# Performance work log

Hardware: AMD Instinct MI355X
Metric: run time of the kernel (lower is better)

Reference implementation:

```python
import jax, jax.numpy as jnp
import numpy as np

B, S, D = 2, 1024, 4096          # batch, prefill seqlen, model dim
H, KVH, HD = 32, 8, 128          # q heads, kv heads, head dim
MAX = 2048                       # kv-cache capacity
THETA = 1000000.0
REP = H // KVH


def _rope_tables(pos):
    # pos: [S] int -> cos/sin [S, HD]
    inv_freq = 1.0 / (THETA ** (jnp.arange(0, HD, 2, dtype=jnp.float32) / HD))
    freqs = pos[:, None].astype(jnp.float32) * inv_freq[None, :]
    emb = jnp.concatenate([freqs, freqs], axis=-1)
    return jnp.cos(emb), jnp.sin(emb)


def _rotate_half(t):
    t1, t2 = jnp.split(t, 2, axis=-1)
    return jnp.concatenate([-t2, t1], axis=-1)


def setup_inputs() -> dict:
    key = jax.random.key(0)
    k = jax.random.split(key, 8)
    sc = 1.0 / np.sqrt(D)
    x = jax.random.normal(k[0], (B, S, D), jnp.float32)
    storage_idx = jnp.arange(S, dtype=jnp.int32)
    cache = jnp.zeros((2, 1, B, KVH, MAX, HD), jnp.float32)
    causal = jnp.tril(jnp.ones((MAX, MAX), bool))
    mask = jnp.where(causal, 0.0, -1e9).astype(jnp.float32)
    Wq = jax.random.normal(k[1], (D, H * HD), jnp.float32) * sc
    bq = jax.random.normal(k[2], (H * HD,), jnp.float32) * 0.01
    Wk = jax.random.normal(k[3], (D, KVH * HD), jnp.float32) * sc
    bk = jax.random.normal(k[4], (KVH * HD,), jnp.float32) * 0.01
    Wv = jax.random.normal(k[5], (D, KVH * HD), jnp.float32) * sc
    bv = jax.random.normal(k[6], (KVH * HD,), jnp.float32) * 0.01
    Wo = jax.random.normal(k[7], (H * HD, D), jnp.float32) * sc
    return {"x": x, "storage_idx": storage_idx, "cache": cache, "mask": mask,
            "Wq": Wq, "bq": bq, "Wk": Wk, "bk": bk, "Wv": Wv, "bv": bv, "Wo": Wo}


def reference(x, storage_idx, cache, mask, Wq, bq, Wk, bk, Wv, bv, Wo):
    bsz, seqlen, _ = x.shape
    # QKV projections -> [b, heads, s, hd]
    xq = (x @ Wq + bq).reshape(bsz, seqlen, H, HD).transpose(0, 2, 1, 3)
    xk = (x @ Wk + bk).reshape(bsz, seqlen, KVH, HD).transpose(0, 2, 1, 3)
    xv = (x @ Wv + bv).reshape(bsz, seqlen, KVH, HD).transpose(0, 2, 1, 3)
    # inline RoPE at positions storage_idx
    cos, sin = _rope_tables(storage_idx)       # [s, hd]
    cos = cos[None, None]                      # [1,1,s,hd]
    sin = sin[None, None]
    xq = xq * cos + _rotate_half(xq) * sin
    xk = xk * cos + _rotate_half(xk) * sin
    # KV-cache scatter (index_copy_ on dim -2 at storage_idx)
    keys = cache[0, 0].at[:, :, storage_idx, :].set(xk)    # [b, kvh, MAX, hd]
    values = cache[1, 0].at[:, :, storage_idx, :].set(xv)
    # GQA: repeat kv heads
    keys = jnp.repeat(keys, REP, axis=1)       # [b, H, MAX, hd]
    values = jnp.repeat(values, REP, axis=1)
    # attention with additive mask rows gathered at storage_idx
    scores = jnp.einsum('bhqd,bhkd->bhqk', xq, keys) / np.sqrt(HD)
    scores = scores + mask[storage_idx][None, None]        # [b, H, s, MAX]
    attn = jax.nn.softmax(scores, axis=-1)
    out = jnp.einsum('bhqk,bhkd->bhqd', attn, values)
    out = out.transpose(0, 2, 1, 3).reshape(bsz, seqlen, H * HD)
    return out @ Wo
```

## Files before the change

kernel.cpp:

```cpp
#include <hip/hip_runtime.h>
#include <hip/hip_bf16.h>

typedef unsigned short u16;
typedef unsigned int   u32;
using bf16x8 = __attribute__((ext_vector_type(8))) short;
using f32x4  = __attribute__((ext_vector_type(4))) float;

#define AS1 __attribute__((address_space(1)))
#define AS3 __attribute__((address_space(3)))

static constexpr int S_   = 1024;
static constexpr int D_   = 4096;
static constexpr int H_   = 32;
static constexpr int KVH_ = 8;
static constexpr int HD_  = 128;
static constexpr int NQKV = H_*HD_ + 2*KVH_*HD_;

__device__ __forceinline__ u16 f2bf(float f) {
  union { float f; u32 u; } v; v.f = f;
  u32 r = v.u + 0x7FFFu + ((v.u >> 16) & 1u);
  return (u16)(r >> 16);
}

__global__ void k_convert(const float* __restrict__ src, u16* __restrict__ dst, int n4) {
  int i = blockIdx.x * blockDim.x + threadIdx.x;
  if (i >= n4) return;
  float4 v = ((const float4*)src)[i];
  ushort4 o;
  o.x = f2bf(v.x); o.y = f2bf(v.y); o.z = f2bf(v.z); o.w = f2bf(v.w);
  ((ushort4*)dst)[i] = o;
}

__global__ void k_transpose_w(const float* __restrict__ src, u16* __restrict__ dst,
                              int K, int N) {
  __shared__ float t[32][33];
  int k0 = blockIdx.y * 32, n0 = blockIdx.x * 32;
  int tx = threadIdx.x, ty = threadIdx.y;
#pragma unroll
  for (int i = 0; i < 4; ++i)
    t[ty + i*8][tx] = src[(size_t)(k0 + ty + i*8) * N + n0 + tx];
  __syncthreads();
#pragma unroll
  for (int i = 0; i < 4; ++i)
    dst[(size_t)(n0 + ty + i*8) * K + k0 + tx] = f2bf(t[tx][ty + i*8]);
}

__global__ void k_transpose_v(const u16* __restrict__ src, u16* __restrict__ dst) {
  __shared__ u16 t[32][33];
  int bg = blockIdx.z;
  int s0 = blockIdx.x * 32, h0 = blockIdx.y * 32;
  src += (size_t)bg * S_ * HD_;
  dst += (size_t)bg * S_ * HD_;
  int tx = threadIdx.x, ty = threadIdx.y;
#pragma unroll
  for (int i = 0; i < 4; ++i)
    t[ty + i*8][tx] = src[(size_t)(s0 + ty + i*8) * HD_ + h0 + tx];
  __syncthreads();
#pragma unroll
  for (int i = 0; i < 4; ++i)
    dst[(size_t)(h0 + ty + i*8) * S_ + s0 + tx] = t[tx][ty + i*8];
}

__global__ void k_rope(const int* __restrict__ sidx, float* __restrict__ cosd,
                       float* __restrict__ sind) {
  int i = blockIdx.x * blockDim.x + threadIdx.x;
  int s = i >> 6, d = i & 63;
  float pos  = (float)sidx[s];
  float invf = expf(-0.21586735246819178f * (float)d);
  float ph   = pos * invf;
  cosd[i] = cosf(ph);
  sind[i] = sinf(ph);
}

__global__ __launch_bounds__(512, 2) void k_gemmq(
    const u16* __restrict__ A, const u16* __restrict__ Bt,
    const float* __restrict__ bq, const float* __restrict__ bk,
    const float* __restrict__ bv,
    const float* __restrict__ cosd, const float* __restrict__ sind,
    u16* __restrict__ qb, u16* __restrict__ kb, u16* __restrict__ vb)
{
  constexpr int K = 4096;
  constexpr int ABYT = 256*128, BBYT = 256*128, STEP = ABYT+BBYT;
  __shared__ __align__(16) char lds[2*STEP];

  const int cpx = (int)gridDim.x >> 3;
  const int wkid = ((int)blockIdx.x & 7)*cpx + ((int)blockIdx.x >> 3);
  const int NT = 24;
  const int m0 = (wkid / NT) * 256, n0 = (wkid % NT) * 256;
  const int tid = threadIdx.x, w = tid>>6, lane = tid&63;
  const int l15 = lane&15, l4 = lane>>4;
  const int wr = w>>1, wc = w&1;
  const int row0 = tid>>3;
  const int ss = (tid&7) ^ (row0&7);
  const int NK = K >> 6;

  f32x4 acc[4][8];
#pragma unroll
  for (int i = 0; i < 4; ++i)
#pragma unroll
    for (int j = 0; j < 8; ++j) acc[i][j] = (f32x4){0.f,0.f,0.f,0.f};

  bf16x8 af[2][2];
  bf16x8 bfr[2][4][2];

#define QCHUNK(kt_, part_, r0c_)                                              \
  __builtin_amdgcn_global_load_lds(                                           \
    (AS1 void*)(((part_) ? Bt + (size_t)(n0 + (r0c_) + row0)*K                \
                         : A  + (size_t)(m0 + (r0c_) + row0)*K)               \
                + (size_t)(kt_)*64 + ss*8),                                   \
    (AS3 void*)(lds + ((kt_)&1)*STEP + (part_)*ABYT + (r0c_)*128 + w*1024),   \
    16, 0, 0)

#define QLOAD_A(mh_)                                                          \
  _Pragma("unroll") for (int i2 = 0; i2 < 2; ++i2)                            \
  _Pragma("unroll") for (int kk = 0; kk < 2; ++kk) {                          \
    int row = wr*64 + ((mh_)*2 + i2)*16 + l15;                                \
    af[i2][kk] = *(const bf16x8*)(lA + row*128 + (((kk*4+l4) ^ (row&7)) << 4)); }

#define QLOAD_B(nh_)                                                          \
  _Pragma("unroll") for (int jj = 0; jj < 4; ++jj)                            \
  _Pragma("unroll") for (int kk = 0; kk < 2; ++kk) {                          \
    int row = wc*128 + ((nh_)*4 + jj)*16 + l15;                               \
    bfr[nh_][jj][kk] = *(const bf16x8*)(lB + row*128 + (((kk*4+l4) ^ (row&7)) << 4)); }

#define QMFMA(mh_, nh_)                                                       \
  __builtin_amdgcn_s_setprio(1);                                              \
  _Pragma("unroll") for (int i2 = 0; i2 < 2; ++i2)                            \
  _Pragma("unroll") for (int jj = 0; jj < 4; ++jj)                            \
  _Pragma("unroll") for (int kk = 0; kk < 2; ++kk)                            \
    acc[(mh_)*2+i2][(nh_)*4+jj] = __builtin_amdgcn_mfma_f32_16x16x32_bf16(    \
        af[i2][kk], bfr[nh_][jj][kk], acc[(mh_)*2+i2][(nh_)*4+jj], 0, 0, 0);  \
  __builtin_amdgcn_s_setprio(0);

#define BAR   __builtin_amdgcn_s_barrier()
#define SCHB  __builtin_amdgcn_sched_barrier(0)
#define WLGKM asm volatile("s_waitcnt lgkmcnt(0)" ::: "memory")

  QCHUNK(0,0,0); QCHUNK(0,0,64); QCHUNK(0,0,128); QCHUNK(0,0,192);
  QCHUNK(0,1,0); QCHUNK(0,1,64); QCHUNK(0,1,128); QCHUNK(0,1,192);
  QCHUNK(1,0,0); QCHUNK(1,0,64); QCHUNK(1,0,128); QCHUNK(1,0,192);
  QCHUNK(1,1,0); QCHUNK(1,1,64); QCHUNK(1,1,128); QCHUNK(1,1,192);
  asm volatile("s_waitcnt vmcnt(8)" ::: "memory");
  BAR; SCHB;

  for (int kt = 0; kt < NK; ++kt) {
    const char* lA = lds + (kt&1)*STEP;
    const char* lB = lA + ABYT;
    QLOAD_A(0); QLOAD_B(0);
    BAR; WLGKM; SCHB;
    QMFMA(0,0);
    BAR;
    QLOAD_B(1);
    BAR; WLGKM; SCHB;
    QMFMA(0,1);
    BAR;
    QLOAD_A(1);
    if (kt+2 < NK) { QCHUNK(kt+2,1,0); QCHUNK(kt+2,1,64); QCHUNK(kt+2,1,128); QCHUNK(kt+2,1,192); }
    BAR; WLGKM; SCHB;
    QMFMA(1,0);
    BAR;
    if (kt+2 < NK) {
      QCHUNK(kt+2,0,0); QCHUNK(kt+2,0,64); QCHUNK(kt+2,0,128); QCHUNK(kt+2,0,192);
      asm volatile("s_waitcnt vmcnt(8)" ::: "memory");
    } else {
      asm volatile("s_waitcnt vmcnt(0)" ::: "memory");
    }
    BAR; WLGKM; SCHB;
    QMFMA(1,1);
    BAR;
  }
#undef QCHUNK
#undef QLOAD_A
#undef QLOAD_B
#undef QMFMA

  const int btype = (n0 >= H_*HD_) + (n0 >= H_*HD_ + KVH_*HD_);
  const int colbase = n0 + wc*128 - (btype==1 ? H_*HD_ : btype==2 ? H_*HD_+KVH_*HD_ : 0);
  const int hloc = colbase >> 7;
  const float* bias = btype==0 ? bq : btype==1 ? bk : bv;
  u16* dst = btype==0 ? qb : btype==1 ? kb : vb;
  const int nheads = btype==0 ? H_ : KVH_;
  const float scale = btype==0 ? 0.08838834764831845f : 1.0f;

  float bb[8];
#pragma unroll
  for (int j = 0; j < 8; ++j) bb[j] = bias[colbase + j*16 + l15];

#pragma unroll
  for (int i = 0; i < 4; ++i)
#pragma unroll
    for (int r = 0; r < 4; ++r) {
      int sr = m0 + wr*64 + i*16 + l4*4 + r;
      int b_ = sr >> 10, s_ = sr & 1023;
      size_t obase = (((size_t)b_*nheads + hloc)*S_ + s_)*(size_t)HD_;
      if (btype < 2) {
#pragma unroll
        for (int j = 0; j < 4; ++j) {
          float cs = cosd[s_*64 + j*16 + l15];
          float sn = sind[s_*64 + j*16 + l15];
          float lo = acc[i][j][r]   + bb[j];
          float hi = acc[i][j+4][r] + bb[j+4];
          dst[obase + j*16 + l15]      = f2bf((lo*cs - hi*sn) * scale);
          dst[obase + 64 + j*16 + l15] = f2bf((hi*cs + lo*sn) * scale);
        }
      } else {
#pragma unroll
        for (int j = 0; j < 8; ++j)
          dst[obase + j*16 + l15] = f2bf(acc[i][j][r] + bb[j]);
      }
    }
}

template<int BN>
__global__ __launch_bounds__(512, 2) void k_gemm3(
    const u16* __restrict__ A, const u16* __restrict__ Bt,
    float* __restrict__ C, int N, int K)
{
  constexpr int WN = BN/4, NJ = WN/16, NH = NJ/2;
  constexpr int ABYT = 256*128, BBYT = BN*128, STEP = ABYT+BBYT;
  __shared__ __align__(16) char lds[2*STEP];

  const int cpx = (int)gridDim.x >> 3;
  const int wkid = ((int)blockIdx.x & 7)*cpx + ((int)blockIdx.x >> 3);
  const int NT = N / BN;
  const int m0 = (wkid / NT) * 256, n0 = (wkid % NT) * BN;
  const int tid = threadIdx.x, w = tid>>6, lane = tid&63;
  const int l15 = lane&15, l4 = lane>>4;
  const int wr = w>>2, wc = w&3;
  const int row0 = tid>>3;
  const int ss = (tid&7) ^ (row0&7);
  const int NK = K >> 6;

  f32x4 acc[8][NJ];
#pragma unroll
  for (int i = 0; i < 8; ++i)
#pragma unroll
    for (int j = 0; j < NJ; ++j) acc[i][j] = (f32x4){0.f,0.f,0.f,0.f};

  bf16x8 af[4][2];
  bf16x8 bf[2][NH][2];

#define CHUNK(kt_, part_, r0c_)                                               \
  __builtin_amdgcn_global_load_lds(                                           \
    (AS1 void*)(((part_) ? Bt + (size_t)(n0 + (r0c_) + row0)*K                \
                         : A  + (size_t)(m0 + (r0c_) + row0)*K)               \
                + (size_t)(kt_)*64 + ss*8),                                   \
    (AS3 void*)(lds + ((kt_)&1)*STEP + (part_)*ABYT + (r0c_)*128 + w*1024),   \
    16, 0, 0)

#define LOAD_A(mh_)                                                           \
  _Pragma("unroll") for (int i = 0; i < 4; ++i)                               \
  _Pragma("unroll") for (int kk = 0; kk < 2; ++kk) {                          \
    int row = wr*128 + (mh_)*64 + i*16 + l15;                                 \
    af[i][kk] = *(const bf16x8*)(lA + row*128 + (((kk*4+l4) ^ (row&7)) << 4)); }

#define LOAD_B(nh_)                                                           \
  _Pragma("unroll") for (int jj = 0; jj < NH; ++jj)                           \
  _Pragma("unroll") for (int kk = 0; kk < 2; ++kk) {                          \
    int row = wc*WN + ((nh_)*NH + jj)*16 + l15;                               \
    bf[nh_][jj][kk] = *(const bf16x8*)(lB + row*128 + (((kk*4+l4) ^ (row&7)) << 4)); }

#define MFMA_PH(mh_, nh_)                                                     \
  __builtin_amdgcn_s_setprio(1);                                              \
  _Pragma("unroll") for (int i = 0; i < 4; ++i)                               \
  _Pragma("unroll") for (int jj = 0; jj < NH; ++jj)                           \
  _Pragma("unroll") for (int kk = 0; kk < 2; ++kk)                            \
    acc[(mh_)*4+i][(nh_)*NH+jj] = __builtin_amdgcn_mfma_f32_16x16x32_bf16(    \
        af[i][kk], bf[nh_][jj][kk], acc[(mh_)*4+i][(nh_)*NH+jj], 0, 0, 0);    \
  __builtin_amdgcn_s_setprio(0);

  CHUNK(0,0,0); CHUNK(0,0,64); CHUNK(0,0,128); CHUNK(0,0,192);
  CHUNK(0,1,0); CHUNK(0,1,64);
  if constexpr (BN == 256) { CHUNK(0,1,128); CHUNK(0,1,192); }
  CHUNK(1,0,0); CHUNK(1,0,128);
  asm volatile("s_waitcnt vmcnt(2)" ::: "memory");
  BAR; SCHB;

  for (int kt = 0; kt < NK; ++kt) {
    const char* lA = lds + (kt&1)*STEP;
    const char* lB = lA + ABYT;
    LOAD_A(0); LOAD_B(0);
    if (kt+1 < NK) { CHUNK(kt+1,0,64); CHUNK(kt+1,0,192); }
    BAR; WLGKM; SCHB;
    MFMA_PH(0,0);
    BAR;
    LOAD_B(1);
    if (kt+1 < NK) {
      CHUNK(kt+1,1,0); CHUNK(kt+1,1,64);
      if constexpr (BN == 256) { CHUNK(kt+1,1,128); CHUNK(kt+1,1,192); }
    }
    BAR; WLGKM; SCHB;
    MFMA_PH(0,1);
    BAR;
    LOAD_A(1);
    if (kt+2 < NK) { CHUNK(kt+2,0,0); CHUNK(kt+2,0,128); }
    BAR; WLGKM; SCHB;
    MFMA_PH(1,0);
    BAR;
    if (kt+2 < NK) asm volatile("s_waitcnt vmcnt(2)" ::: "memory");
    else           asm volatile("s_waitcnt vmcnt(0)" ::: "memory");
    BAR; WLGKM; SCHB;
    MFMA_PH(1,1);
    BAR;
  }
#undef CHUNK
#undef LOAD_A
#undef LOAD_B
#undef MFMA_PH

#pragma unroll
  for (int i = 0; i < 8; ++i)
#pragma unroll
    for (int j = 0; j < NJ; ++j) {
      int r0 = m0 + wr*128 + i*16 + l4*4;
      int c0 = n0 + wc*WN + j*16 + l15;
#pragma unroll
      for (int r = 0; r < 4; ++r)
        C[(size_t)(r0 + r) * N + c0] = acc[i][j][r];
    }
}

__global__ __launch_bounds__(256, 4) void k_attn(
    const u16* __restrict__ Q, const u16* __restrict__ Kc,
    const u16* __restrict__ Vt, const u16* __restrict__ AOdummy, u16* __restrict__ AO)
{
  __shared__ __align__(16) char Kls[2][16384];
  __shared__ __align__(16) char Vls[2][16384];
  __shared__ u16 Pl[4][1024];

  int id = blockIdx.x;
  int slot = id >> 3;
  int bg   = (id & 7)*2 + (slot & 1);
  int rem  = slot >> 1;
  int h_in = rem & 3, bx = rem >> 2;
  int b = bg >> 3, g = bg & 7, h = g*4 + h_in;
  int tA = bx, tB = 15 - bx;

  int tid = threadIdx.x, w = tid >> 6, lane = tid & 63;
  int l15 = lane & 15, l4 = lane >> 4;
  const u16* Qh = Q  + ((size_t)b*H_   + h) * S_ * HD_;
  const u16* Kp = Kc + ((size_t)b*KVH_ + g) * S_ * HD_;
  const u16* Vp = Vt + ((size_t)b*KVH_ + g) * (size_t)HD_ * S_;
  u16* AOh = AO + ((size_t)b*S_) * (H_*HD_) + h*HD_;
  char* Pw = (char*)&Pl[w][0];

  int kOff[4], vOff[4];
#pragma unroll
  for (int c = 0; c < 4; ++c) {
    int ci = c*256 + tid;
    int krow = ci >> 4, ks = ci & 15;
    kOff[c] = krow * HD_ + ((ks & 8) | ((ks & 7) ^ (krow & 7))) * 8;
    int vrow = ci >> 3, vs = ci & 7;
    vOff[c] = vrow * S_ + (vs ^ (vrow & 7)) * 8;
  }

#define ASTAGE(kv_, bb_) {                                                    \
    const u16* ks_ = Kp + (size_t)(kv_) * 64 * HD_;                           \
    const u16* vs_ = Vp + (size_t)(kv_) * 64;                                 \
    _Pragma("unroll") for (int c = 0; c < 4; ++c) {                           \
      __builtin_amdgcn_global_load_lds((AS1 void*)(ks_ + kOff[c]),            \
          (AS3 void*)(&Kls[bb_][0] + c*4096 + w*1024), 16, 0, 0);             \
      __builtin_amdgcn_global_load_lds((AS1 void*)(vs_ + vOff[c]),            \
          (AS3 void*)(&Vls[bb_][0] + c*4096 + w*1024), 16, 0, 0); } }

  bf16x8 qf[4];
#pragma unroll
  for (int kc = 0; kc < 4; ++kc)
    qf[kc] = *(const bf16x8*)(Qh + (size_t)(tA*64 + w*16 + l15)*HD_ + kc*32 + l4*8);

  f32x4 o[8];
#pragma unroll
  for (int n = 0; n < 8; ++n) o[n] = (f32x4){0.f,0.f,0.f,0.f};
  float mrow[4] = {-3e38f,-3e38f,-3e38f,-3e38f};
  float lrow[4] = {0.f,0.f,0.f,0.f};

  ASTAGE(0, 0);
  asm volatile("s_waitcnt vmcnt(0)" ::: "memory");
  __builtin_amdgcn_s_barrier();

  const int NIT = tA + tB + 2;
  int buf = 0;
  for (int it = 0; it < NIT; ++it) {
    bool phA = (it <= tA);
    int kv = phA ? it : it - tA - 1;
    int qt = phA ? tA : tB;
    if (it + 1 < NIT) {
      int kvn = (it + 1 <= tA) ? it + 1 : it - tA;
      ASTAGE(kvn, buf ^ 1);
    }
    const char* Ksb = &Kls[buf][0];
    const char* Vsb = &Vls[buf][0];

    f32x4 sc[4];
    __builtin_amdgcn_s_setprio(1);
#pragma unroll
    for (int ct = 0; ct < 4; ++ct) {
      f32x4 s4 = (f32x4){0.f,0.f,0.f,0.f};
#pragma unroll
      for (int kc = 0; kc < 4; ++kc) {
        int row = ct*16 + l15, s = kc*4 + l4;
        bf16x8 kf = *(const bf16x8*)(Ksb + row*256 + ((((s & 7) ^ (row & 7)) | (s & 8)) << 4));
        s4 = __builtin_amdgcn_mfma_f32_16x16x32_bf16(qf[kc], kf, s4, 0, 0, 0);
      }
      sc[ct] = s4;
    }
    __builtin_amdgcn_s_setprio(0);

    if (kv == qt) {
      int qrow0 = qt*64 + w*16;
#pragma unroll
      for (int ct = 0; ct < 4; ++ct)
#pragma unroll
        for (int r = 0; r < 4; ++r) {
          int col = kv*64 + ct*16 + l15;
          if (col > qrow0 + l4*4 + r) sc[ct][r] = -1e9f;
        }
    }

    float f[4];
#pragma unroll
    for (int r = 0; r < 4; ++r) {
      float mx = fmaxf(fmaxf(sc[0][r], sc[1][r]), fmaxf(sc[2][r], sc[3][r]));
      mx = fmaxf(mx, __shfl_xor(mx, 1));
      mx = fmaxf(mx, __shfl_xor(mx, 2));
      mx = fmaxf(mx, __shfl_xor(mx, 4));
      mx = fmaxf(mx, __shfl_xor(mx, 8));
      float nm = fmaxf(mrow[r], mx);
      f[r] = __expf(mrow[r] - nm);
      mrow[r] = nm;
    }
    float rs[4] = {0.f,0.f,0.f,0.f};
#pragma unroll
    for (int ct = 0; ct < 4; ++ct)
#pragma unroll
      for (int r = 0; r < 4; ++r) {
        float p = __expf(sc[ct][r] - mrow[r]);
        rs[r] += p;
        int row = l4*4 + r, col = ct*16 + l15;
        int byte = row*128 + (((col >> 3) ^ (row & 7)) << 4) + (col & 7)*2;
        *(u16*)(Pw + byte) = f2bf(p);
      }
#pragma unroll
    for (int r = 0; r < 4; ++r) {
      float sum = rs[r];
      sum += __shfl_xor(sum, 1);
      sum += __shfl_xor(sum, 2);
      sum += __shfl_xor(sum, 4);
      sum += __shfl_xor(sum, 8);
      lrow[r] = lrow[r]*f[r] + sum;
    }
#pragma unroll
    for (int n = 0; n < 8; ++n)
#pragma unroll
      for (int r = 0; r < 4; ++r) o[n][r] *= f[r];

    __builtin_amdgcn_s_setprio(1);
#pragma unroll
    for (int kk = 0; kk < 2; ++kk) {
      int pbyte = l15*128 + (((kk*4 + l4) ^ (l15 & 7)) << 4);
      bf16x8 pf = *(const bf16x8*)(Pw + pbyte);
#pragma unroll
      for (int n = 0; n < 8; ++n) {
        int vrow = n*16 + l15, s = kk*4 + l4;
        bf16x8 vf = *(const bf16x8*)(Vsb + vrow*128 + ((s ^ (vrow & 7)) << 4));
        o[n] = __builtin_amdgcn_mfma_f32_16x16x32_bf16(pf, vf, o[n], 0, 0, 0);
      }
    }
    __builtin_amdgcn_s_setprio(0);

    if (it == tA) {
#pragma unroll
      for (int n = 0; n < 8; ++n)
#pragma unroll
        for (int r = 0; r < 4; ++r) {
          int srow = tA*64 + w*16 + l4*4 + r;
          AOh[(size_t)srow * (H_*HD_) + n*16 + l15] = f2bf(o[n][r] / lrow[r]);
        }
#pragma unroll
      for (int n = 0; n < 8; ++n) o[n] = (f32x4){0.f,0.f,0.f,0.f};
#pragma unroll
      for (int r = 0; r < 4; ++r) { mrow[r] = -3e38f; lrow[r] = 0.f; }
#pragma unroll
      for (int kc = 0; kc < 4; ++kc)
        qf[kc] = *(const bf16x8*)(Qh + (size_t)(tB*64 + w*16 + l15)*HD_ + kc*32 + l4*8);
    }

    asm volatile("s_waitcnt vmcnt(0)" ::: "memory");
    __builtin_amdgcn_s_barrier();
    buf ^= 1;
  }
#undef ASTAGE

#pragma unroll
  for (int n = 0; n < 8; ++n)
#pragma unroll
    for (int r = 0; r < 4; ++r) {
      int srow = tB*64 + w*16 + l4*4 + r;
      AOh[(size_t)srow * (H_*HD_) + n*16 + l15] = f2bf(o[n][r] / lrow[r]);
    }
}

extern "C" void kernel_launch(void* const* d_in, const int* in_sizes, int n_in,
                              void* d_out, int out_size, void* d_ws, size_t ws_size,
                              hipStream_t stream) {
  (void)in_sizes; (void)n_in; (void)out_size; (void)ws_size;
  const float* x   = (const float*)d_in[0];
  const int*   sid = (const int*)  d_in[1];
  const float* Wq  = (const float*)d_in[4];
  const float* bq  = (const float*)d_in[5];
  const float* Wk  = (const float*)d_in[6];
  const float* bk  = (const float*)d_in[7];
  const float* Wv  = (const float*)d_in[8];
  const float* bv  = (const float*)d_in[9];
  const float* Wo  = (const float*)d_in[10];
  float* out = (float*)d_out;

  char* ws = (char*)d_ws;
  u16*   xb   = (u16*)  (ws);
  u16*   WB   = (u16*)  (ws + 16777216);
  u16*   WoT  = (u16*)  (ws + 67108864);
  u16*   qb   = (u16*)  (ws + 150994944);
  u16*   kb   = (u16*)  (ws + 167772160);
  u16*   vb   = (u16*)  (ws + 171966464);
  u16*   VT   = (u16*)  (ws + 176160768);
  float* cosd = (float*)(ws + 180355072);
  float* sind = (float*)(ws + 180617216);
  u16*   AO   = xb;

  dim3 tb(32, 8);
  k_convert<<<8192, 256, 0, stream>>>(x, xb, (2048*4096)/4);
  k_transpose_w<<<dim3(128,128), tb, 0, stream>>>(Wq, WB, 4096, 4096);
  k_transpose_w<<<dim3( 32,128), tb, 0, stream>>>(Wk, WB + (size_t)4096*4096, 4096, 1024);
  k_transpose_w<<<dim3( 32,128), tb, 0, stream>>>(Wv, WB + (size_t)5120*4096, 4096, 1024);
  k_transpose_w<<<dim3(128,128), tb, 0, stream>>>(Wo, WoT, 4096, 4096);
  k_rope<<<256, 256, 0, stream>>>(sid, cosd, sind);
  k_gemmq<<<192, 512, 0, stream>>>(xb, WB, bq, bk, bv, cosd, sind, qb, kb, vb);
  k_transpose_v<<<dim3(32,4,16), tb, 0, stream>>>(vb, VT);
  k_attn<<<512, 256, 0, stream>>>(qb, kb, VT, qb, AO);
  k_gemm3<128><<<256, 512, 0, stream>>>(AO, WoT, out, 4096, 4096);
}
```

Measured before the change: 315.0 us.

## Software-pipeline LDS fragment reads across MFMA phases in both GEMMs

```diff
diff --git a/kernel.cpp b/kernel.cpp
--- a/kernel.cpp
+++ b/kernel.cpp
@@ -71,6 +71,9 @@
   cosd[i] = cosf(ph);
   sind[i] = sinf(ph);
 }
+
+#define BAR   __builtin_amdgcn_s_barrier()
+#define SCHB  __builtin_amdgcn_sched_barrier(0)
 
 __global__ __launch_bounds__(512, 2) void k_gemmq(
     const u16* __restrict__ A, const u16* __restrict__ Bt,
@@ -100,7 +103,7 @@
 #pragma unroll
     for (int j = 0; j < 8; ++j) acc[i][j] = (f32x4){0.f,0.f,0.f,0.f};
 
-  bf16x8 af[2][2];
+  bf16x8 af[2][2][2];
   bf16x8 bfr[2][4][2];
 
 #define QCHUNK(kt_, part_, r0c_)                                              \
@@ -111,17 +114,17 @@
     (AS3 void*)(lds + ((kt_)&1)*STEP + (part_)*ABYT + (r0c_)*128 + w*1024),   \
     16, 0, 0)
 
-#define QLOAD_A(mh_)                                                          \
+#define QR_A(mh_, lA_)                                                        \
   _Pragma("unroll") for (int i2 = 0; i2 < 2; ++i2)                            \
   _Pragma("unroll") for (int kk = 0; kk < 2; ++kk) {                          \
     int row = wr*64 + ((mh_)*2 + i2)*16 + l15;                                \
-    af[i2][kk] = *(const bf16x8*)(lA + row*128 + (((kk*4+l4) ^ (row&7)) << 4)); }
-
-#define QLOAD_B(nh_)                                                          \
+    af[mh_][i2][kk] = *(const bf16x8*)((lA_) + row*128 + (((kk*4+l4) ^ (row&7)) << 4)); }
+
+#define QR_B(nh_, lB_)                                                        \
   _Pragma("unroll") for (int jj = 0; jj < 4; ++jj)                            \
   _Pragma("unroll") for (int kk = 0; kk < 2; ++kk) {                          \
     int row = wc*128 + ((nh_)*4 + jj)*16 + l15;                               \
-    bfr[nh_][jj][kk] = *(const bf16x8*)(lB + row*128 + (((kk*4+l4) ^ (row&7)) << 4)); }
+    bfr[nh_][jj][kk] = *(const bf16x8*)((lB_) + row*128 + (((kk*4+l4) ^ (row&7)) << 4)); }
 
 #define QMFMA(mh_, nh_)                                                       \
   __builtin_amdgcn_s_setprio(1);                                              \
@@ -129,12 +132,8 @@
   _Pragma("unroll") for (int jj = 0; jj < 4; ++jj)                            \
   _Pragma("unroll") for (int kk = 0; kk < 2; ++kk)                            \
     acc[(mh_)*2+i2][(nh_)*4+jj] = __builtin_amdgcn_mfma_f32_16x16x32_bf16(    \
-        af[i2][kk], bfr[nh_][jj][kk], acc[(mh_)*2+i2][(nh_)*4+jj], 0, 0, 0);  \
+        af[mh_][i2][kk], bfr[nh_][jj][kk], acc[(mh_)*2+i2][(nh_)*4+jj], 0, 0, 0); \
   __builtin_amdgcn_s_setprio(0);
-
-#define BAR   __builtin_amdgcn_s_barrier()
-#define SCHB  __builtin_amdgcn_sched_barrier(0)
-#define WLGKM asm volatile("s_waitcnt lgkmcnt(0)" ::: "memory")
 
   QCHUNK(0,0,0); QCHUNK(0,0,64); QCHUNK(0,0,128); QCHUNK(0,0,192);
   QCHUNK(0,1,0); QCHUNK(0,1,64); QCHUNK(0,1,128); QCHUNK(0,1,192);
@@ -142,36 +141,42 @@
   QCHUNK(1,1,0); QCHUNK(1,1,64); QCHUNK(1,1,128); QCHUNK(1,1,192);
   asm volatile("s_waitcnt vmcnt(8)" ::: "memory");
   BAR; SCHB;
+  {
+    const char* lA0 = lds;
+    const char* lB0 = lds + ABYT;
+    QR_A(0, lA0); QR_B(0, lB0);
+  }
 
   for (int kt = 0; kt < NK; ++kt) {
     const char* lA = lds + (kt&1)*STEP;
     const char* lB = lA + ABYT;
-    QLOAD_A(0); QLOAD_B(0);
-    BAR; WLGKM; SCHB;
+    QR_B(1, lB);
+    asm volatile("s_waitcnt lgkmcnt(8)" ::: "memory");
+    SCHB;
     QMFMA(0,0);
-    BAR;
-    QLOAD_B(1);
-    BAR; WLGKM; SCHB;
+    QR_A(1, lA);
+    asm volatile("s_waitcnt lgkmcnt(4)" ::: "memory");
+    BAR; SCHB;
+    if (kt+2 < NK) { QCHUNK(kt+2,1,0); QCHUNK(kt+2,1,64); QCHUNK(kt+2,1,128); QCHUNK(kt+2,1,192); }
     QMFMA(0,1);
-    BAR;
-    QLOAD_A(1);
-    if (kt+2 < NK) { QCHUNK(kt+2,1,0); QCHUNK(kt+2,1,64); QCHUNK(kt+2,1,128); QCHUNK(kt+2,1,192); }
-    BAR; WLGKM; SCHB;
+    asm volatile("s_waitcnt lgkmcnt(0)" ::: "memory");
+    BAR; SCHB;
+    if (kt+2 < NK) { QCHUNK(kt+2,0,0); QCHUNK(kt+2,0,64); QCHUNK(kt+2,0,128); QCHUNK(kt+2,0,192); }
     QMFMA(1,0);
-    BAR;
-    if (kt+2 < NK) {
-      QCHUNK(kt+2,0,0); QCHUNK(kt+2,0,64); QCHUNK(kt+2,0,128); QCHUNK(kt+2,0,192);
-      asm volatile("s_waitcnt vmcnt(8)" ::: "memory");
-    } else {
-      asm volatile("s_waitcnt vmcnt(0)" ::: "memory");
-    }
-    BAR; WLGKM; SCHB;
+    if (kt+1 < NK) {
+      if (kt+2 < NK) asm volatile("s_waitcnt vmcnt(8)" ::: "memory");
+      else           asm volatile("s_waitcnt vmcnt(0)" ::: "memory");
+      BAR; SCHB;
+      const char* lAn = lds + ((kt+1)&1)*STEP;
+      const char* lBn = lAn + ABYT;
+      QR_A(0, lAn); QR_B(0, lBn);
+      SCHB;
+    }
     QMFMA(1,1);
-    BAR;
   }
 #undef QCHUNK
-#undef QLOAD_A
-#undef QLOAD_B
+#undef QR_A
+#undef QR_B
 #undef QMFMA
 
   const int btype = (n0 >= H_*HD_) + (n0 >= H_*HD_ + KVH_*HD_);
@@ -211,19 +216,17 @@
     }
 }
 
-template<int BN>
-__global__ __launch_bounds__(512, 2) void k_gemm3(
+__global__ __launch_bounds__(512, 2) void k_gemmo(
     const u16* __restrict__ A, const u16* __restrict__ Bt,
     float* __restrict__ C, int N, int K)
 {
-  constexpr int WN = BN/4, NJ = WN/16, NH = NJ/2;
-  constexpr int ABYT = 256*128, BBYT = BN*128, STEP = ABYT+BBYT;
+  constexpr int ABYT = 256*128, BBYT = 128*128, STEP = ABYT+BBYT;
   __shared__ __align__(16) char lds[2*STEP];
 
   const int cpx = (int)gridDim.x >> 3;
   const int wkid = ((int)blockIdx.x & 7)*cpx + ((int)blockIdx.x >> 3);
-  const int NT = N / BN;
-  const int m0 = (wkid / NT) * 256, n0 = (wkid % NT) * BN;
+  const int NT = N / 128;
+  const int m0 = (wkid / NT) * 256, n0 = (wkid % NT) * 128;
   const int tid = threadIdx.x, w = tid>>6, lane = tid&63;
   const int l15 = lane&15, l4 = lane>>4;
   const int wr = w>>2, wc = w&3;
@@ -231,16 +234,16 @@
   const int ss = (tid&7) ^ (row0&7);
   const int NK = K >> 6;
 
-  f32x4 acc[8][NJ];
+  f32x4 acc[8][2];
 #pragma unroll
   for (int i = 0; i < 8; ++i)
 #pragma unroll
-    for (int j = 0; j < NJ; ++j) acc[i][j] = (f32x4){0.f,0.f,0.f,0.f};
-
-  bf16x8 af[4][2];
-  bf16x8 bf[2][NH][2];
-
-#define CHUNK(kt_, part_, r0c_)                                               \
+    for (int j = 0; j < 2; ++j) acc[i][j] = (f32x4){0.f,0.f,0.f,0.f};
+
+  bf16x8 af[2][4][2];
+  bf16x8 bfr[2][2];
+
+#define OCHUNK(kt_, part_, r0c_)                                              \
   __builtin_amdgcn_global_load_lds(                                           \
     (AS1 void*)(((part_) ? Bt + (size_t)(n0 + (r0c_) + row0)*K                \
                          : A  + (size_t)(m0 + (r0c_) + row0)*K)               \
@@ -248,72 +251,75 @@
     (AS3 void*)(lds + ((kt_)&1)*STEP + (part_)*ABYT + (r0c_)*128 + w*1024),   \
     16, 0, 0)
 
-#define LOAD_A(mh_)                                                           \
+#define OR_A(mh_, lA_)                                                        \
   _Pragma("unroll") for (int i = 0; i < 4; ++i)                               \
   _Pragma("unroll") for (int kk = 0; kk < 2; ++kk) {                          \
-    int row = wr*128 + (mh_)*64 + i*16 + l15;                                 \
-    af[i][kk] = *(const bf16x8*)(lA + row*128 + (((kk*4+l4) ^ (row&7)) << 4)); }
-
-#define LOAD_B(nh_)                                                           \
-  _Pragma("unroll") for (int jj = 0; jj < NH; ++jj)                           \
+    int row = wr*128 + ((mh_)*4 + i)*16 + l15;                                \
+    af[mh_][i][kk] = *(const bf16x8*)((lA_) + row*128 + (((kk*4+l4) ^ (row&7)) << 4)); }
+
+#define OR_B(nh_, lB_)                                                        \
   _Pragma("unroll") for (int kk = 0; kk < 2; ++kk) {                          \
-    int row = wc*WN + ((nh_)*NH + jj)*16 + l15;                               \
-    bf[nh_][jj][kk] = *(const bf16x8*)(lB + row*128 + (((kk*4+l4) ^ (row&7)) << 4)); }
-
-#define MFMA_PH(mh_, nh_)                                                     \
+    int row = wc*32 + (nh_)*16 + l15;                                         \
+    bfr[nh_][kk] = *(const bf16x8*)((lB_) + row*128 + (((kk*4+l4) ^ (row&7)) << 4)); }
+
+#define OMFMA(mh_, nh_)                                                       \
   __builtin_amdgcn_s_setprio(1);                                              \
   _Pragma("unroll") for (int i = 0; i < 4; ++i)                               \
-  _Pragma("unroll") for (int jj = 0; jj < NH; ++jj)                           \
   _Pragma("unroll") for (int kk = 0; kk < 2; ++kk)                            \
-    acc[(mh_)*4+i][(nh_)*NH+jj] = __builtin_amdgcn_mfma_f32_16x16x32_bf16(    \
-        af[i][kk], bf[nh_][jj][kk], acc[(mh_)*4+i][(nh_)*NH+jj], 0, 0, 0);    \
+    acc[(mh_)*4+i][nh_] = __builtin_amdgcn_mfma_f32_16x16x32_bf16(            \
+        af[mh_][i][kk], bfr[nh_][kk], acc[(mh_)*4+i][nh_], 0, 0, 0);          \
   __builtin_amdgcn_s_setprio(0);
 
-  CHUNK(0,0,0); CHUNK(0,0,64); CHUNK(0,0,128); CHUNK(0,0,192);
-  CHUNK(0,1,0); CHUNK(0,1,64);
-  if constexpr (BN == 256) { CHUNK(0,1,128); CHUNK(0,1,192); }
-  CHUNK(1,0,0); CHUNK(1,0,128);
-  asm volatile("s_waitcnt vmcnt(2)" ::: "memory");
+  OCHUNK(0,0,0); OCHUNK(0,0,64); OCHUNK(0,0,128); OCHUNK(0,0,192);
+  OCHUNK(0,1,0); OCHUNK(0,1,64);
+  OCHUNK(1,0,0); OCHUNK(1,0,64); OCHUNK(1,0,128); OCHUNK(1,0,192);
+  OCHUNK(1,1,0); OCHUNK(1,1,64);
+  asm volatile("s_waitcnt vmcnt(6)" ::: "memory");
   BAR; SCHB;
+  {
+    const char* lA0 = lds;
+    const char* lB0 = lds + ABYT;
+    OR_A(0, lA0); OR_B(0, lB0);
+  }
 
   for (int kt = 0; kt < NK; ++kt) {
     const char* lA = lds + (kt&1)*STEP;
     const char* lB = lA + ABYT;
-    LOAD_A(0); LOAD_B(0);
-    if (kt+1 < NK) { CHUNK(kt+1,0,64); CHUNK(kt+1,0,192); }
-    BAR; WLGKM; SCHB;
-    MFMA_PH(0,0);
-    BAR;
-    LOAD_B(1);
+    OR_B(1, lB);
+    asm volatile("s_waitcnt lgkmcnt(2)" ::: "memory");
+    SCHB;
+    OMFMA(0,0);
+    OR_A(1, lA);
+    asm volatile("s_waitcnt lgkmcnt(8)" ::: "memory");
+    BAR; SCHB;
+    if (kt+2 < NK) { OCHUNK(kt+2,1,0); OCHUNK(kt+2,1,64); }
+    OMFMA(0,1);
+    asm volatile("s_waitcnt lgkmcnt(0)" ::: "memory");
+    BAR; SCHB;
+    if (kt+2 < NK) { OCHUNK(kt+2,0,0); OCHUNK(kt+2,0,64); OCHUNK(kt+2,0,128); OCHUNK(kt+2,0,192); }
+    OMFMA(1,0);
     if (kt+1 < NK) {
-      CHUNK(kt+1,1,0); CHUNK(kt+1,1,64);
-      if constexpr (BN == 256) { CHUNK(kt+1,1,128); CHUNK(kt+1,1,192); }
-    }
-    BAR; WLGKM; SCHB;
-    MFMA_PH(0,1);
-    BAR;
-    LOAD_A(1);
-    if (kt+2 < NK) { CHUNK(kt+2,0,0); CHUNK(kt+2,0,128); }
-    BAR; WLGKM; SCHB;
-    MFMA_PH(1,0);
-    BAR;
-    if (kt+2 < NK) asm volatile("s_waitcnt vmcnt(2)" ::: "memory");
-    else           asm volatile("s_waitcnt vmcnt(0)" ::: "memory");
-    BAR; WLGKM; SCHB;
-    MFMA_PH(1,1);
-    BAR;
+      if (kt+2 < NK) asm volatile("s_waitcnt vmcnt(6)" ::: "memory");
+      else           asm volatile("s_waitcnt vmcnt(0)" ::: "memory");
+      BAR; SCHB;
+      const char* lAn = lds + ((kt+1)&1)*STEP;
+      const char* lBn = lAn + ABYT;
+      OR_A(0, lAn); OR_B(0, lBn);
+      SCHB;
+    }
+    OMFMA(1,1);
   }
-#undef CHUNK
-#undef LOAD_A
-#undef LOAD_B
-#undef MFMA_PH
+#undef OCHUNK
+#undef OR_A
+#undef OR_B
+#undef OMFMA
 
 #pragma unroll
   for (int i = 0; i < 8; ++i)
 #pragma unroll
-    for (int j = 0; j < NJ; ++j) {
+    for (int j = 0; j < 2; ++j) {
       int r0 = m0 + wr*128 + i*16 + l4*4;
-      int c0 = n0 + wc*WN + j*16 + l15;
+      int c0 = n0 + wc*32 + j*16 + l15;
 #pragma unroll
       for (int r = 0; r < 4; ++r)
         C[(size_t)(r0 + r) * N + c0] = acc[i][j][r];
@@ -322,7 +328,7 @@
 
 __global__ __launch_bounds__(256, 4) void k_attn(
     const u16* __restrict__ Q, const u16* __restrict__ Kc,
-    const u16* __restrict__ Vt, const u16* __restrict__ AOdummy, u16* __restrict__ AO)
+    const u16* __restrict__ Vt, u16* __restrict__ AO)
 {
   __shared__ __align__(16) char Kls[2][16384];
   __shared__ __align__(16) char Vls[2][16384];
@@ -536,6 +542,6 @@
   k_rope<<<256, 256, 0, stream>>>(sid, cosd, sind);
   k_gemmq<<<192, 512, 0, stream>>>(xb, WB, bq, bk, bv, cosd, sind, qb, kb, vb);
   k_transpose_v<<<dim3(32,4,16), tb, 0, stream>>>(vb, VT);
-  k_attn<<<512, 256, 0, stream>>>(qb, kb, VT, qb, AO);
-  k_gemm3<128><<<256, 512, 0, stream>>>(AO, WoT, out, 4096, 4096);
-}
+  k_attn<<<512, 256, 0, stream>>>(qb, kb, VT, AO);
+  k_gemmo<<<256, 512, 0, stream>>>(AO, WoT, out, 4096, 4096);
+}
```

Measured after the change: 294.0 us. -6.7%, faster.
